# Performance work log

Hardware: AMD Instinct MI355X
Metric: run time of the kernel (lower is better)

## Reference

```python
import jax, jax.numpy as jnp
import numpy as np

B, S, D, H, MLP_D = 2, 2048, 512, 8, 128
DH = D // H  # 64
EPS = 1e-5


def setup_inputs() -> dict:
    key = jax.random.key(0)
    ks = jax.random.split(key, 8)
    return {
        "z": jax.random.normal(ks[0], (B, S, D), dtype=jnp.float32),
        "head_w": jax.random.normal(ks[1], (H, D, 3 * DH), dtype=jnp.float32),
        "w_o": jax.random.normal(ks[2], (H * DH, D), dtype=jnp.float32),
        "ln_w": jnp.ones((D,), dtype=jnp.float32),
        "ln_b": jnp.zeros((D,), dtype=jnp.float32),
        "w1": jax.random.normal(ks[3], (D, MLP_D), dtype=jnp.float32) * (1.0 / np.sqrt(D)),
        "b1": jnp.zeros((MLP_D,), dtype=jnp.float32),
        "w2": jax.random.normal(ks[4], (MLP_D, D), dtype=jnp.float32) * (1.0 / np.sqrt(MLP_D)),
        "b2": jnp.zeros((D,), dtype=jnp.float32),
    }


def _layernorm(x, w, b):
    mu = jnp.mean(x, axis=-1, keepdims=True)
    var = jnp.var(x, axis=-1, keepdims=True)
    return (x - mu) * jax.lax.rsqrt(var + EPS) * w + b


def reference(z, head_w, w_o, ln_w, ln_b, w1, b1, w2, b2):
    # --- MSA block: z = MSA(LN(z)) + z ---
    x = _layernorm(z, ln_w, ln_b)                       # [B,S,D]
    qkv = jnp.einsum("bsd,hde->bhse", x, head_w)        # [B,H,S,3*DH]
    q, k, v = qkv[..., :DH], qkv[..., DH:2 * DH], qkv[..., 2 * DH:]
    scores = jnp.einsum("bhsd,bhtd->bhst", q, k) / jnp.sqrt(jnp.float32(DH))
    p = jax.nn.softmax(scores, axis=-1)                 # [B,H,S,S]
    o = jnp.einsum("bhst,bhtd->bhsd", p, v)             # [B,H,S,DH]
    # concat heads along last dim (head order matches torch.cat), then project
    o = jnp.transpose(o, (0, 2, 1, 3)).reshape(B, S, H * DH)
    z = o @ w_o + z
    # --- MLP block: z = GELU(Linear2(Linear1(LN(z)))) + z (GELU last, per Sequential) ---
    y = _layernorm(z, ln_w, ln_b)
    y = (y @ w1 + b1) @ w2 + b2
    z = jax.nn.gelu(y, approximate=False) + z
    return z
```

## Files before the change

kernel.cpp:

```cpp
#include <hip/hip_runtime.h>
#include <hip/hip_bf16.h>

typedef unsigned short u16;
typedef __attribute__((ext_vector_type(8))) short short8;
typedef __attribute__((ext_vector_type(8))) __bf16 bf16x8;
typedef __attribute__((ext_vector_type(4))) float f32x4;

#define DEV static __device__ __forceinline__

DEV float bf2f(u16 u) { unsigned v = ((unsigned)u) << 16; float f; __builtin_memcpy(&f, &v, 4); return f; }
DEV u16 f2bf(float f) {
  unsigned u; __builtin_memcpy(&u, &f, 4);
  unsigned lsb = (u >> 16) & 1;
  u += 0x7fffu + lsb;
  return (u16)(u >> 16);
}
DEV u16 tbf(float f) {
  unsigned u; __builtin_memcpy(&u, &f, 4);
  return (u16)(u >> 16);
}
DEV float exp2fast(float x) { return __builtin_amdgcn_exp2f(x); }
DEV f32x4 mfma16(short8 a, short8 b, f32x4 c) {
  return __builtin_amdgcn_mfma_f32_16x16x32_bf16(
      __builtin_bit_cast(bf16x8, a), __builtin_bit_cast(bf16x8, b), c, 0, 0, 0);
}
DEV short8 ld8(const u16* p) { return *(const short8*)p; }

__global__ void prep_all(const float* __restrict__ hw, const float* __restrict__ wo,
                         const float* __restrict__ w1, const float* __restrict__ w2,
                         u16* __restrict__ wqh, u16* __restrict__ wql,
                         u16* __restrict__ woT, u16* __restrict__ w1T, u16* __restrict__ w2T) {
  int idx = blockIdx.x * 256 + threadIdx.x;
  if (idx < 786432) {
    int e = idx % 192;
    int d = (idx / 192) % 512;
    int h = idx / (192 * 512);
    float v = hw[idx];
    int n = (e < 64) ? (h * 64 + e) : (e < 128) ? (512 + h * 64 + e - 64) : (1024 + h * 64 + e - 128);
    size_t oi = (size_t)n * 512 + d;
    u16 hh = f2bf(v);
    wqh[oi] = hh;
    if (e < 128) wql[oi] = f2bf(v - bf2f(hh));
  } else if (idx < 786432 + 262144) {
    int i = idx - 786432;
    int n = i % 512, k = i / 512;
    woT[(size_t)n * 512 + k] = f2bf(wo[i]);
  } else if (idx < 786432 + 262144 + 65536) {
    int i = idx - (786432 + 262144);
    int n = i % 128, k = i / 128;
    w1T[(size_t)n * 512 + k] = f2bf(w1[i]);
  } else if (idx < 786432 + 262144 + 131072) {
    int i = idx - (786432 + 262144 + 65536);
    int n = i % 512, k = i / 512;
    w2T[(size_t)n * 128 + k] = f2bf(w2[i]);
  }
}

__global__ __launch_bounds__(256) void ln_kernel(const float* __restrict__ in,
                                                 const float* __restrict__ w,
                                                 const float* __restrict__ bb,
                                                 u16* __restrict__ hi, u16* __restrict__ lo) {
  const int wv = threadIdx.x >> 6, lane = threadIdx.x & 63;
  const int row = blockIdx.x * 4 + wv;
  const float4* r = (const float4*)(in + (size_t)row * 512);
  float4 a0 = r[lane * 2], a1 = r[lane * 2 + 1];
  float s = a0.x + a0.y + a0.z + a0.w + a1.x + a1.y + a1.z + a1.w;
  float ss = a0.x * a0.x + a0.y * a0.y + a0.z * a0.z + a0.w * a0.w +
             a1.x * a1.x + a1.y * a1.y + a1.z * a1.z + a1.w * a1.w;
#pragma unroll
  for (int m = 1; m < 64; m <<= 1) { s += __shfl_xor(s, m); ss += __shfl_xor(ss, m); }
  float mu = s * (1.f / 512.f);
  float var = ss * (1.f / 512.f) - mu * mu;
  float rstd = rsqrtf(var + 1e-5f);
  const float4* wp = (const float4*)w + lane * 2;
  const float4* bp = (const float4*)bb + lane * 2;
  float4 w0 = wp[0], w1v = wp[1], b0 = bp[0], b1v = bp[1];
  float xv[8] = {a0.x, a0.y, a0.z, a0.w, a1.x, a1.y, a1.z, a1.w};
  float wv8[8] = {w0.x, w0.y, w0.z, w0.w, w1v.x, w1v.y, w1v.z, w1v.w};
  float bv8[8] = {b0.x, b0.y, b0.z, b0.w, b1v.x, b1v.y, b1v.z, b1v.w};
  short8 oh, ol;
#pragma unroll
  for (int i = 0; i < 8; i++) {
    float v = (xv[i] - mu) * rstd * wv8[i] + bv8[i];
    u16 hh = f2bf(v);
    oh[i] = (short)hh;
    ol[i] = (short)f2bf(v - bf2f(hh));
  }
  *(short8*)(hi + (size_t)row * 512 + lane * 8) = oh;
  *(short8*)(lo + (size_t)row * 512 + lane * 8) = ol;
}

__global__ __launch_bounds__(256) void gemm_qkv(const u16* __restrict__ Ah, const u16* __restrict__ Alo,
                                                const u16* __restrict__ Bh, const u16* __restrict__ Blo,
                                                u16* __restrict__ outh, u16* __restrict__ outl) {
  __shared__ __align__(16) u16 As[128][40], Asl[128][40], Bs[64][40], Bsl[64][40];
  const int tid = threadIdx.x, lane = tid & 63, wv = tid >> 6;
  const int wm = wv >> 1, wn = wv & 1, g = lane >> 4, r16 = lane & 15;
  const int bm = blockIdx.x * 128, bn = blockIdx.y * 64;
  const bool split = blockIdx.y < 16;
  short8 sA[2], sAl[2], sB, sBl;
  auto ldtile = [&](int kt) {
#pragma unroll
    for (int c = 0; c < 2; c++) {
      int ch = c * 256 + tid;
      sA[c] = ld8(Ah + (size_t)(bm + (ch >> 2)) * 512 + kt + (ch & 3) * 8);
      if (split) sAl[c] = ld8(Alo + (size_t)(bm + (ch >> 2)) * 512 + kt + (ch & 3) * 8);
    }
    sB = ld8(Bh + (size_t)(bn + (tid >> 2)) * 512 + kt + (tid & 3) * 8);
    if (split) sBl = ld8(Blo + (size_t)(bn + (tid >> 2)) * 512 + kt + (tid & 3) * 8);
  };
  f32x4 acc[4][2] = {};
  ldtile(0);
  for (int kt = 0; kt < 512; kt += 32) {
    __syncthreads();
#pragma unroll
    for (int c = 0; c < 2; c++) {
      int ch = c * 256 + tid;
      *(short8*)&As[ch >> 2][(ch & 3) * 8] = sA[c];
      if (split) *(short8*)&Asl[ch >> 2][(ch & 3) * 8] = sAl[c];
    }
    *(short8*)&Bs[tid >> 2][(tid & 3) * 8] = sB;
    if (split) *(short8*)&Bsl[tid >> 2][(tid & 3) * 8] = sBl;
    __syncthreads();
    if (kt + 32 < 512) ldtile(kt + 32);
    short8 af[4], bf_[2], afl[4], bfl[2];
#pragma unroll
    for (int mi = 0; mi < 4; mi++) af[mi] = *(const short8*)&As[wm * 64 + mi * 16 + r16][g * 8];
#pragma unroll
    for (int ni = 0; ni < 2; ni++) bf_[ni] = *(const short8*)&Bs[wn * 32 + ni * 16 + r16][g * 8];
    if (split) {
#pragma unroll
      for (int mi = 0; mi < 4; mi++) afl[mi] = *(const short8*)&Asl[wm * 64 + mi * 16 + r16][g * 8];
#pragma unroll
      for (int ni = 0; ni < 2; ni++) bfl[ni] = *(const short8*)&Bsl[wn * 32 + ni * 16 + r16][g * 8];
    }
#pragma unroll
    for (int mi = 0; mi < 4; mi++)
#pragma unroll
      for (int ni = 0; ni < 2; ni++) {
        acc[mi][ni] = mfma16(af[mi], bf_[ni], acc[mi][ni]);
        if (split) {
          acc[mi][ni] = mfma16(af[mi], bfl[ni], acc[mi][ni]);
          acc[mi][ni] = mfma16(afl[mi], bf_[ni], acc[mi][ni]);
        }
      }
  }
#pragma unroll
  for (int mi = 0; mi < 4; mi++)
#pragma unroll
    for (int ni = 0; ni < 2; ni++) {
      int col = bn + wn * 32 + ni * 16 + r16;
      int row0 = bm + wm * 64 + mi * 16 + g * 4;
#pragma unroll
      for (int j = 0; j < 4; j++) {
        size_t oi = (size_t)(row0 + j) * 1536 + col;
        float v = acc[mi][ni][j];
        u16 hh = f2bf(v);
        outh[oi] = hh;
        if (split) outl[oi] = f2bf(v - bf2f(hh));
      }
    }
}

template <int MF, int NF, int EPI>
__global__ __launch_bounds__(256) void gemm_g(const u16* __restrict__ A, const u16* __restrict__ BT,
                                              const float* __restrict__ res, const float* __restrict__ bias,
                                              u16* __restrict__ outb, float* __restrict__ outf,
                                              int N, int K) {
  constexpr int BM = 32 * MF, BN = 32 * NF;
  constexpr int CA = (BM * 4 + 255) / 256, CB = (BN * 4 + 255) / 256;
  __shared__ __align__(16) u16 As[BM][40], Bs[BN][40];
  const int tid = threadIdx.x, lane = tid & 63, wv = tid >> 6;
  const int wm = wv >> 1, wn = wv & 1, g = lane >> 4, r16 = lane & 15;
  const int bm = blockIdx.x * BM, bn = blockIdx.y * BN;
  short8 sA[CA], sB[CB];
  auto ldtile = [&](int kt) {
#pragma unroll
    for (int c = 0; c < CA; c++) {
      int ch = c * 256 + tid;
      if (ch < BM * 4) sA[c] = ld8(A + (size_t)(bm + (ch >> 2)) * K + kt + (ch & 3) * 8);
    }
#pragma unroll
    for (int c = 0; c < CB; c++) {
      int ch = c * 256 + tid;
      if (ch < BN * 4) sB[c] = ld8(BT + (size_t)(bn + (ch >> 2)) * K + kt + (ch & 3) * 8);
    }
  };
  f32x4 acc[MF][NF] = {};
  ldtile(0);
  for (int kt = 0; kt < K; kt += 32) {
    __syncthreads();
#pragma unroll
    for (int c = 0; c < CA; c++) {
      int ch = c * 256 + tid;
      if (ch < BM * 4) *(short8*)&As[ch >> 2][(ch & 3) * 8] = sA[c];
    }
#pragma unroll
    for (int c = 0; c < CB; c++) {
      int ch = c * 256 + tid;
      if (ch < BN * 4) *(short8*)&Bs[ch >> 2][(ch & 3) * 8] = sB[c];
    }
    __syncthreads();
    if (kt + 32 < K) ldtile(kt + 32);
    short8 af[MF], bf_[NF];
#pragma unroll
    for (int mi = 0; mi < MF; mi++) af[mi] = *(const short8*)&As[wm * 16 * MF + mi * 16 + r16][g * 8];
#pragma unroll
    for (int ni = 0; ni < NF; ni++) bf_[ni] = *(const short8*)&Bs[wn * 16 * NF + ni * 16 + r16][g * 8];
#pragma unroll
    for (int mi = 0; mi < MF; mi++)
#pragma unroll
      for (int ni = 0; ni < NF; ni++) acc[mi][ni] = mfma16(af[mi], bf_[ni], acc[mi][ni]);
  }
#pragma unroll
  for (int mi = 0; mi < MF; mi++)
#pragma unroll
    for (int ni = 0; ni < NF; ni++) {
      int col = bn + wn * 16 * NF + ni * 16 + r16;
      int row0 = bm + wm * 16 * MF + mi * 16 + g * 4;
#pragma unroll
      for (int j = 0; j < 4; j++) {
        size_t oi = (size_t)(row0 + j) * N + col;
        float v = acc[mi][ni][j];
        if (EPI == 1) {
          outf[oi] = v + res[oi];
        } else if (EPI == 2) {
          outb[oi] = f2bf(v + bias[col]);
        } else {
          float u = v + bias[col];
          float gl = 0.5f * u * (1.0f + erff(u * 0.70710678118f));
          outf[oi] = gl + res[oi];
        }
      }
    }
}

__global__ __launch_bounds__(256) void attn_kernel(const u16* __restrict__ qkv_hi,
                                                   const u16* __restrict__ qkv_lo,
                                                   u16* __restrict__ o) {
  constexpr int SK = 72, SV = 136, SP = 136;
  __shared__ __align__(16) u16 Kh[128 * SK], Kl[128 * SK], Vt[64 * SV];
  __shared__ __align__(16) u16 Pl[4][16 * SP];
  const int tid = threadIdx.x, lane = tid & 63, w = tid >> 6;
  const int g = lane >> 4, r16 = lane & 15;
  const int qb = blockIdx.x * 64;
  const int b = blockIdx.y >> 3, h = blockIdx.y & 7;
  const size_t bbase = (size_t)b * 2048 * 1536;
  const u16* Qh = qkv_hi + bbase + h * 64;
  const u16* Ql = qkv_lo + bbase + h * 64;
  const u16* KgH = qkv_hi + bbase + 512 + h * 64;
  const u16* KgL = qkv_lo + bbase + 512 + h * 64;
  const u16* Vg = qkv_hi + bbase + 1024 + h * 64;

  const int qrow = qb + w * 16 + r16;
  short8 qh[2], qlo[2];
#pragma unroll
  for (int ks = 0; ks < 2; ks++) {
    qh[ks] = ld8(Qh + (size_t)qrow * 1536 + ks * 32 + g * 8);
    qlo[ks] = ld8(Ql + (size_t)qrow * 1536 + ks * 32 + g * 8);
  }

  f32x4 oacc[4] = {};
  float m_r[4], l_r[4];
#pragma unroll
  for (int j = 0; j < 4; j++) { m_r[j] = -3e38f; l_r[j] = 0.f; }

  short8 kA[4], kB[4], vS[4];
  auto ldkv = [&](int kt) {
#pragma unroll
    for (int c = 0; c < 4; c++) {
      int ch = c * 256 + tid;
      int kr = ch >> 3, kc = (ch & 7) * 8;
      kA[c] = ld8(KgH + (size_t)(kt + kr) * 1536 + kc);
      kB[c] = ld8(KgL + (size_t)(kt + kr) * 1536 + kc);
    }
#pragma unroll
    for (int c = 0; c < 2; c++)
#pragma unroll
      for (int c2 = 0; c2 < 2; c2++)
        vS[c * 2 + c2] = ld8(Vg + (size_t)(kt + c * 64 + lane) * 1536 + w * 16 + c2 * 8);
  };
  ldkv(0);

  for (int kt = 0; kt < 2048; kt += 128) {
    __syncthreads();
#pragma unroll
    for (int c = 0; c < 4; c++) {
      int ch = c * 256 + tid;
      int kr = ch >> 3, kc = (ch & 7) * 8;
      *(short8*)&Kh[kr * SK + kc] = kA[c];
      *(short8*)&Kl[kr * SK + kc] = kB[c];
    }
#pragma unroll
    for (int c = 0; c < 2; c++)
#pragma unroll
      for (int c2 = 0; c2 < 2; c2++)
#pragma unroll
        for (int i = 0; i < 8; i++)
          Vt[(w * 16 + c2 * 8 + i) * SV + c * 64 + lane] = (u16)vS[c * 2 + c2][i];
    __syncthreads();
    if (kt + 128 < 2048) ldkv(kt + 128);
    f32x4 s[8];
#pragma unroll
    for (int f = 0; f < 8; f++) {
      s[f] = f32x4{0.f, 0.f, 0.f, 0.f};
#pragma unroll
      for (int ks = 0; ks < 2; ks++) {
        short8 bh = *(const short8*)&Kh[(f * 16 + r16) * SK + ks * 32 + g * 8];
        short8 bl = *(const short8*)&Kl[(f * 16 + r16) * SK + ks * 32 + g * 8];
        s[f] = mfma16(qh[ks], bh, s[f]);
        s[f] = mfma16(qh[ks], bl, s[f]);
        s[f] = mfma16(qlo[ks], bh, s[f]);
      }
    }
    constexpr float SCL2 = 0.125f * 1.44269504f;
    float scl[4];
#pragma unroll
    for (int j = 0; j < 4; j++) {
      float a[8];
#pragma unroll
      for (int f = 0; f < 8; f++) a[f] = s[f][j] * SCL2;
      float vm = fmaxf(fmaxf(fmaxf(a[0], a[1]), fmaxf(a[2], a[3])),
                       fmaxf(fmaxf(a[4], a[5]), fmaxf(a[6], a[7])));
      vm = fmaxf(vm, __shfl_xor(vm, 1));
      vm = fmaxf(vm, __shfl_xor(vm, 2));
      vm = fmaxf(vm, __shfl_xor(vm, 4));
      vm = fmaxf(vm, __shfl_xor(vm, 8));
      float mn = fmaxf(m_r[j], vm);
      float rs = 0.f;
      int pr = (g * 4 + j) * SP + r16;
#pragma unroll
      for (int f = 0; f < 8; f++) {
        float e = exp2fast(a[f] - mn);
        rs += e;
        Pl[w][pr + f * 16] = tbf(e);
      }
      rs += __shfl_xor(rs, 1);
      rs += __shfl_xor(rs, 2);
      rs += __shfl_xor(rs, 4);
      rs += __shfl_xor(rs, 8);
      scl[j] = exp2fast(m_r[j] - mn);
      m_r[j] = mn;
      l_r[j] = l_r[j] * scl[j] + rs;
    }
#pragma unroll
    for (int dt = 0; dt < 4; dt++)
#pragma unroll
      for (int j = 0; j < 4; j++) oacc[dt][j] *= scl[j];
#pragma unroll
    for (int ks = 0; ks < 4; ks++) {
      short8 pa = *(const short8*)&Pl[w][r16 * SP + ks * 32 + g * 8];
#pragma unroll
      for (int dt = 0; dt < 4; dt++) {
        short8 vb = *(const short8*)&Vt[(dt * 16 + r16) * SV + ks * 32 + g * 8];
        oacc[dt] = mfma16(pa, vb, oacc[dt]);
      }
    }
  }
  float il[4];
#pragma unroll
  for (int j = 0; j < 4; j++) il[j] = 1.f / l_r[j];
#pragma unroll
  for (int dt = 0; dt < 4; dt++)
#pragma unroll
    for (int j = 0; j < 4; j++) {
      int row = b * 2048 + qb + w * 16 + g * 4 + j;
      int col = h * 64 + dt * 16 + r16;
      o[(size_t)row * 512 + col] = f2bf(oacc[dt][j] * il[j]);
    }
}

extern "C" void kernel_launch(void* const* d_in, const int* in_sizes, int n_in,
                              void* d_out, int out_size, void* d_ws, size_t ws_size,
                              hipStream_t stream) {
  const float* z = (const float*)d_in[0];
  const float* head_w = (const float*)d_in[1];
  const float* w_o = (const float*)d_in[2];
  const float* ln_w = (const float*)d_in[3];
  const float* ln_b = (const float*)d_in[4];
  const float* w1 = (const float*)d_in[5];
  const float* b1 = (const float*)d_in[6];
  const float* w2 = (const float*)d_in[7];
  const float* b2 = (const float*)d_in[8];
  float* out = (float*)d_out;

  size_t off = 0;
  auto alc = [&](size_t n) {
    void* p = (char*)d_ws + off;
    off += (n + 255) & ~(size_t)255;
    return p;
  };
  u16* x_hi = (u16*)alc((size_t)4096 * 512 * 2);
  u16* x_lo = (u16*)alc((size_t)4096 * 512 * 2);
  u16* wqh = (u16*)alc((size_t)1536 * 512 * 2);
  u16* wql = (u16*)alc((size_t)1536 * 512 * 2);
  u16* woT = (u16*)alc((size_t)512 * 512 * 2);
  u16* w1T = (u16*)alc((size_t)128 * 512 * 2);
  u16* w2T = (u16*)alc((size_t)512 * 128 * 2);
  u16* qkvh = (u16*)alc((size_t)4096 * 1536 * 2);
  u16* qkvl = (u16*)alc((size_t)4096 * 1536 * 2);
  u16* ob = (u16*)alc((size_t)4096 * 512 * 2);
  float* z2 = (float*)alc((size_t)4096 * 512 * 4);
  u16* tb = (u16*)alc((size_t)4096 * 128 * 2);

  prep_all<<<4608, 256, 0, stream>>>(head_w, w_o, w1, w2, wqh, wql, woT, w1T, w2T);

  ln_kernel<<<1024, 256, 0, stream>>>(z, ln_w, ln_b, x_hi, x_lo);

  gemm_qkv<<<dim3(32, 24), 256, 0, stream>>>(x_hi, x_lo, wqh, wql, qkvh, qkvl);

  attn_kernel<<<dim3(32, 16), 256, 0, stream>>>(qkvh, qkvl, ob);

  gemm_g<2, 2, 1><<<dim3(64, 8), 256, 0, stream>>>(ob, woT, z, nullptr, nullptr, z2, 512, 512);

  ln_kernel<<<1024, 256, 0, stream>>>(z2, ln_w, ln_b, x_hi, x_lo);

  gemm_g<1, 2, 2><<<dim3(128, 2), 256, 0, stream>>>(x_hi, w1T, nullptr, b1, tb, nullptr, 128, 512);

  gemm_g<2, 2, 3><<<dim3(64, 8), 256, 0, stream>>>(tb, w2T, z2, b2, nullptr, out, 512, 128);
}
```

Before: 144.5 us.

## Split attention KV range across two wave groups per block and merge results

The attention kernel now launches 512 threads per block, and each half of the waves processes half of the key/value sequence with 64-row tiles. At the end, the two partial softmax states are merged through shared memory. This doubles the waves working on each query tile, so more latency can be hidden on a grid of only 512 blocks. The cost is an extra merge step and shared-memory exchange, plus higher register pressure under launch bounds of 512 threads and 4 blocks.

```diff
diff --git a/kernel.cpp b/kernel.cpp
--- a/kernel.cpp
+++ b/kernel.cpp
@@ -235,13 +235,12 @@
     }
 }
 
-__global__ __launch_bounds__(256) void attn_kernel(const u16* __restrict__ qkv_hi,
-                                                   const u16* __restrict__ qkv_lo,
-                                                   u16* __restrict__ o) {
-  constexpr int SK = 72, SV = 136, SP = 136;
-  __shared__ __align__(16) u16 Kh[128 * SK], Kl[128 * SK], Vt[64 * SV];
-  __shared__ __align__(16) u16 Pl[4][16 * SP];
+__global__ __launch_bounds__(512, 4) void attn_kernel(const u16* __restrict__ qkv_hi,
+                                                      const u16* __restrict__ qkv_lo,
+                                                      u16* __restrict__ ob) {
+  __shared__ __align__(16) u16 smem[36864];
   const int tid = threadIdx.x, lane = tid & 63, w = tid >> 6;
+  const int half = w >> 2, wq = w & 3;
   const int g = lane >> 4, r16 = lane & 15;
   const int qb = blockIdx.x * 64;
   const int b = blockIdx.y >> 3, h = blockIdx.y & 7;
@@ -251,8 +250,12 @@
   const u16* KgH = qkv_hi + bbase + 512 + h * 64;
   const u16* KgL = qkv_lo + bbase + 512 + h * 64;
   const u16* Vg = qkv_hi + bbase + 1024 + h * 64;
-
-  const int qrow = qb + w * 16 + r16;
+  u16* Kh = smem + half * 4608;
+  u16* Kl = smem + 9216 + half * 4608;
+  u16* Vt = smem + 18432 + half * 4608;
+  u16* Pw = smem + 27648 + w * 1152;
+
+  const int qrow = qb + wq * 16 + r16;
   short8 qh[2], qlo[2];
 #pragma unroll
   for (int ks = 0; ks < 2; ks++) {
@@ -265,49 +268,44 @@
 #pragma unroll
   for (int j = 0; j < 4; j++) { m_r[j] = -3e38f; l_r[j] = 0.f; }
 
-  short8 kA[4], kB[4], vS[4];
+  const int th = tid & 255;
+  const int sr = th >> 2, sc16 = (th & 3) * 16;
+  const int kv0 = half * 1024;
+  short8 kA[2], kB[2], vS[2];
   auto ldkv = [&](int kt) {
-#pragma unroll
-    for (int c = 0; c < 4; c++) {
-      int ch = c * 256 + tid;
-      int kr = ch >> 3, kc = (ch & 7) * 8;
-      kA[c] = ld8(KgH + (size_t)(kt + kr) * 1536 + kc);
-      kB[c] = ld8(KgL + (size_t)(kt + kr) * 1536 + kc);
-    }
+    const u16* kp = KgH + (size_t)(kt + sr) * 1536 + sc16;
+    const u16* lp = KgL + (size_t)(kt + sr) * 1536 + sc16;
+    kA[0] = ld8(kp);
+    kA[1] = ld8(kp + 8);
+    kB[0] = ld8(lp);
+    kB[1] = ld8(lp + 8);
+    vS[0] = ld8(Vg + (size_t)(kt + lane) * 1536 + wq * 16);
+    vS[1] = ld8(Vg + (size_t)(kt + lane) * 1536 + wq * 16 + 8);
+  };
+  ldkv(kv0);
+
+  for (int kt = kv0; kt < kv0 + 1024; kt += 64) {
+    __syncthreads();
+    *(short8*)&Kh[sr * 72 + sc16] = kA[0];
+    *(short8*)&Kh[sr * 72 + sc16 + 8] = kA[1];
+    *(short8*)&Kl[sr * 72 + sc16] = kB[0];
+    *(short8*)&Kl[sr * 72 + sc16 + 8] = kB[1];
 #pragma unroll
     for (int c = 0; c < 2; c++)
 #pragma unroll
-      for (int c2 = 0; c2 < 2; c2++)
-        vS[c * 2 + c2] = ld8(Vg + (size_t)(kt + c * 64 + lane) * 1536 + w * 16 + c2 * 8);
-  };
-  ldkv(0);
-
-  for (int kt = 0; kt < 2048; kt += 128) {
-    __syncthreads();
-#pragma unroll
-    for (int c = 0; c < 4; c++) {
-      int ch = c * 256 + tid;
-      int kr = ch >> 3, kc = (ch & 7) * 8;
-      *(short8*)&Kh[kr * SK + kc] = kA[c];
-      *(short8*)&Kl[kr * SK + kc] = kB[c];
-    }
-#pragma unroll
-    for (int c = 0; c < 2; c++)
-#pragma unroll
-      for (int c2 = 0; c2 < 2; c2++)
-#pragma unroll
-        for (int i = 0; i < 8; i++)
-          Vt[(w * 16 + c2 * 8 + i) * SV + c * 64 + lane] = (u16)vS[c * 2 + c2][i];
-    __syncthreads();
-    if (kt + 128 < 2048) ldkv(kt + 128);
-    f32x4 s[8];
-#pragma unroll
-    for (int f = 0; f < 8; f++) {
+      for (int i = 0; i < 8; i++)
+        Vt[(wq * 16 + c * 8 + i) * 72 + lane] = (u16)vS[c][i];
+    __syncthreads();
+    if (kt + 64 < kv0 + 1024) ldkv(kt + 64);
+    f32x4 s[4];
+#pragma unroll
+    for (int f = 0; f < 4; f++) {
       s[f] = f32x4{0.f, 0.f, 0.f, 0.f};
+      int krow = f * 16 + r16;
 #pragma unroll
       for (int ks = 0; ks < 2; ks++) {
-        short8 bh = *(const short8*)&Kh[(f * 16 + r16) * SK + ks * 32 + g * 8];
-        short8 bl = *(const short8*)&Kl[(f * 16 + r16) * SK + ks * 32 + g * 8];
+        short8 bh = *(const short8*)&Kh[krow * 72 + ks * 32 + g * 8];
+        short8 bl = *(const short8*)&Kl[krow * 72 + ks * 32 + g * 8];
         s[f] = mfma16(qh[ks], bh, s[f]);
         s[f] = mfma16(qh[ks], bl, s[f]);
         s[f] = mfma16(qlo[ks], bh, s[f]);
@@ -317,24 +315,17 @@
     float scl[4];
 #pragma unroll
     for (int j = 0; j < 4; j++) {
-      float a[8];
-#pragma unroll
-      for (int f = 0; f < 8; f++) a[f] = s[f][j] * SCL2;
-      float vm = fmaxf(fmaxf(fmaxf(a[0], a[1]), fmaxf(a[2], a[3])),
-                       fmaxf(fmaxf(a[4], a[5]), fmaxf(a[6], a[7])));
+      float a0 = s[0][j] * SCL2, a1 = s[1][j] * SCL2;
+      float a2 = s[2][j] * SCL2, a3 = s[3][j] * SCL2;
+      float vm = fmaxf(fmaxf(a0, a1), fmaxf(a2, a3));
       vm = fmaxf(vm, __shfl_xor(vm, 1));
       vm = fmaxf(vm, __shfl_xor(vm, 2));
       vm = fmaxf(vm, __shfl_xor(vm, 4));
       vm = fmaxf(vm, __shfl_xor(vm, 8));
       float mn = fmaxf(m_r[j], vm);
-      float rs = 0.f;
-      int pr = (g * 4 + j) * SP + r16;
-#pragma unroll
-      for (int f = 0; f < 8; f++) {
-        float e = exp2fast(a[f] - mn);
-        rs += e;
-        Pl[w][pr + f * 16] = tbf(e);
-      }
+      float e0 = exp2fast(a0 - mn), e1 = exp2fast(a1 - mn);
+      float e2 = exp2fast(a2 - mn), e3 = exp2fast(a3 - mn);
+      float rs = (e0 + e1) + (e2 + e3);
       rs += __shfl_xor(rs, 1);
       rs += __shfl_xor(rs, 2);
       rs += __shfl_xor(rs, 4);
@@ -342,32 +333,63 @@
       scl[j] = exp2fast(m_r[j] - mn);
       m_r[j] = mn;
       l_r[j] = l_r[j] * scl[j] + rs;
+      int pr = (g * 4 + j) * 72 + r16;
+      Pw[pr] = tbf(e0);
+      Pw[pr + 16] = tbf(e1);
+      Pw[pr + 32] = tbf(e2);
+      Pw[pr + 48] = tbf(e3);
     }
 #pragma unroll
     for (int dt = 0; dt < 4; dt++)
 #pragma unroll
       for (int j = 0; j < 4; j++) oacc[dt][j] *= scl[j];
 #pragma unroll
-    for (int ks = 0; ks < 4; ks++) {
-      short8 pa = *(const short8*)&Pl[w][r16 * SP + ks * 32 + g * 8];
+    for (int ks = 0; ks < 2; ks++) {
+      short8 pa = *(const short8*)&Pw[r16 * 72 + ks * 32 + g * 8];
 #pragma unroll
       for (int dt = 0; dt < 4; dt++) {
-        short8 vb = *(const short8*)&Vt[(dt * 16 + r16) * SV + ks * 32 + g * 8];
+        short8 vb = *(const short8*)&Vt[(dt * 16 + r16) * 72 + ks * 32 + g * 8];
         oacc[dt] = mfma16(pa, vb, oacc[dt]);
       }
     }
   }
-  float il[4];
-#pragma unroll
-  for (int j = 0; j < 4; j++) il[j] = 1.f / l_r[j];
-#pragma unroll
-  for (int dt = 0; dt < 4; dt++)
+  __syncthreads();
+  float* oex = (float*)smem;
+  float* mlx = (float*)(smem + 9216);
+  if (half == 1) {
+#pragma unroll
+    for (int dt = 0; dt < 4; dt++)
+#pragma unroll
+      for (int j = 0; j < 4; j++)
+        oex[(wq * 16 + g * 4 + j) * 68 + dt * 16 + r16] = oacc[dt][j];
+    if (r16 == 0) {
+#pragma unroll
+      for (int j = 0; j < 4; j++) {
+        mlx[(wq * 16 + g * 4 + j) * 2] = m_r[j];
+        mlx[(wq * 16 + g * 4 + j) * 2 + 1] = l_r[j];
+      }
+    }
+  }
+  __syncthreads();
+  if (half == 0) {
 #pragma unroll
     for (int j = 0; j < 4; j++) {
-      int row = b * 2048 + qb + w * 16 + g * 4 + j;
-      int col = h * 64 + dt * 16 + r16;
-      o[(size_t)row * 512 + col] = f2bf(oacc[dt][j] * il[j]);
-    }
+      int rr = wq * 16 + g * 4 + j;
+      float m1 = mlx[rr * 2], l1 = mlx[rr * 2 + 1];
+      float mm = fmaxf(m_r[j], m1);
+      float c0 = exp2fast(m_r[j] - mm), c1 = exp2fast(m1 - mm);
+      float inv = 1.f / (c0 * l_r[j] + c1 * l1);
+      c0 *= inv;
+      c1 *= inv;
+      int row = b * 2048 + qb + rr;
+#pragma unroll
+      for (int dt = 0; dt < 4; dt++) {
+        float o1 = oex[rr * 68 + dt * 16 + r16];
+        int col = h * 64 + dt * 16 + r16;
+        ob[(size_t)row * 512 + col] = f2bf(oacc[dt][j] * c0 + o1 * c1);
+      }
+    }
+  }
 }
 
 extern "C" void kernel_launch(void* const* d_in, const int* in_sizes, int n_in,
@@ -409,7 +431,7 @@
 
   gemm_qkv<<<dim3(32, 24), 256, 0, stream>>>(x_hi, x_lo, wqh, wql, qkvh, qkvl);
 
-  attn_kernel<<<dim3(32, 16), 256, 0, stream>>>(qkvh, qkvl, ob);
+  attn_kernel<<<dim3(32, 16), 512, 0, stream>>>(qkvh, qkvl, ob);
 
   gemm_g<2, 2, 1><<<dim3(64, 8), 256, 0, stream>>>(ob, woT, z, nullptr, nullptr, z2, 512, 512);
 
```

Result: slower. 151.2 us (+4.6%).

## Emit V transposed from QKV GEMM so attention loads it with vector stores

Applied to the files above, without the earlier changes.

The QKV GEMM epilogue now writes Q/K hi/lo into a compact 1024-wide buffer and writes V transposed ([512 dims][4096 tokens]) as packed 4-element stores. The attention kernel then loads V rows contiguously along the key axis and stores them to LDS with 16-byte vector writes, replacing the per-element scatter transpose. This removes scalar LDS writes and strided global loads in the attention inner loop. In exchange, the GEMM writes V with a 4096-element stride between columns, which scatters its stores.

```diff
diff --git a/kernel.cpp b/kernel.cpp
--- a/kernel.cpp
+++ b/kernel.cpp
@@ -92,7 +92,8 @@
 
 __global__ __launch_bounds__(256) void gemm_qkv(const u16* __restrict__ Ah, const u16* __restrict__ Alo,
                                                 const u16* __restrict__ Bh, const u16* __restrict__ Blo,
-                                                u16* __restrict__ outh, u16* __restrict__ outl) {
+                                                u16* __restrict__ qkh, u16* __restrict__ qkl,
+                                                u16* __restrict__ vT) {
   __shared__ __align__(16) u16 As[128][40], Asl[128][40], Bs[64][40], Bsl[64][40];
   const int tid = threadIdx.x, lane = tid & 63, wv = tid >> 6;
   const int wm = wv >> 1, wn = wv & 1, g = lane >> 4, r16 = lane & 15;
@@ -151,13 +152,23 @@
     for (int ni = 0; ni < 2; ni++) {
       int col = bn + wn * 32 + ni * 16 + r16;
       int row0 = bm + wm * 64 + mi * 16 + g * 4;
-#pragma unroll
-      for (int j = 0; j < 4; j++) {
-        size_t oi = (size_t)(row0 + j) * 1536 + col;
-        float v = acc[mi][ni][j];
-        u16 hh = f2bf(v);
-        outh[oi] = hh;
-        if (split) outl[oi] = f2bf(v - bf2f(hh));
+      if (split) {
+#pragma unroll
+        for (int j = 0; j < 4; j++) {
+          size_t oi = (size_t)(row0 + j) * 1024 + col;
+          float v = acc[mi][ni][j];
+          u16 hh = f2bf(v);
+          qkh[oi] = hh;
+          qkl[oi] = f2bf(v - bf2f(hh));
+        }
+      } else {
+        int vcol = col - 1024;
+        ushort4 pk;
+        pk.x = f2bf(acc[mi][ni][0]);
+        pk.y = f2bf(acc[mi][ni][1]);
+        pk.z = f2bf(acc[mi][ni][2]);
+        pk.w = f2bf(acc[mi][ni][3]);
+        *(ushort4*)(vT + (size_t)vcol * 4096 + row0) = pk;
       }
     }
 }
@@ -235,8 +246,9 @@
     }
 }
 
-__global__ __launch_bounds__(256) void attn_kernel(const u16* __restrict__ qkv_hi,
-                                                   const u16* __restrict__ qkv_lo,
+__global__ __launch_bounds__(256) void attn_kernel(const u16* __restrict__ qkh,
+                                                   const u16* __restrict__ qkl,
+                                                   const u16* __restrict__ vT,
                                                    u16* __restrict__ o) {
   constexpr int SK = 72, SV = 136, SP = 136;
   __shared__ __align__(16) u16 Kh[128 * SK], Kl[128 * SK], Vt[64 * SV];
@@ -245,19 +257,19 @@
   const int g = lane >> 4, r16 = lane & 15;
   const int qb = blockIdx.x * 64;
   const int b = blockIdx.y >> 3, h = blockIdx.y & 7;
-  const size_t bbase = (size_t)b * 2048 * 1536;
-  const u16* Qh = qkv_hi + bbase + h * 64;
-  const u16* Ql = qkv_lo + bbase + h * 64;
-  const u16* KgH = qkv_hi + bbase + 512 + h * 64;
-  const u16* KgL = qkv_lo + bbase + 512 + h * 64;
-  const u16* Vg = qkv_hi + bbase + 1024 + h * 64;
+  const size_t bbase = (size_t)b * 2048 * 1024;
+  const u16* Qh = qkh + bbase + h * 64;
+  const u16* Ql = qkl + bbase + h * 64;
+  const u16* KgH = qkh + bbase + 512 + h * 64;
+  const u16* KgL = qkl + bbase + 512 + h * 64;
+  const u16* Vtg = vT + (size_t)h * 64 * 4096 + (size_t)b * 2048;
 
   const int qrow = qb + w * 16 + r16;
   short8 qh[2], qlo[2];
 #pragma unroll
   for (int ks = 0; ks < 2; ks++) {
-    qh[ks] = ld8(Qh + (size_t)qrow * 1536 + ks * 32 + g * 8);
-    qlo[ks] = ld8(Ql + (size_t)qrow * 1536 + ks * 32 + g * 8);
+    qh[ks] = ld8(Qh + (size_t)qrow * 1024 + ks * 32 + g * 8);
+    qlo[ks] = ld8(Ql + (size_t)qrow * 1024 + ks * 32 + g * 8);
   }
 
   f32x4 oacc[4] = {};
@@ -265,20 +277,19 @@
 #pragma unroll
   for (int j = 0; j < 4; j++) { m_r[j] = -3e38f; l_r[j] = 0.f; }
 
+  const int vd0 = tid >> 4, vkv = (tid & 15) * 8;
   short8 kA[4], kB[4], vS[4];
   auto ldkv = [&](int kt) {
 #pragma unroll
     for (int c = 0; c < 4; c++) {
       int ch = c * 256 + tid;
       int kr = ch >> 3, kc = (ch & 7) * 8;
-      kA[c] = ld8(KgH + (size_t)(kt + kr) * 1536 + kc);
-      kB[c] = ld8(KgL + (size_t)(kt + kr) * 1536 + kc);
-    }
-#pragma unroll
-    for (int c = 0; c < 2; c++)
-#pragma unroll
-      for (int c2 = 0; c2 < 2; c2++)
-        vS[c * 2 + c2] = ld8(Vg + (size_t)(kt + c * 64 + lane) * 1536 + w * 16 + c2 * 8);
+      kA[c] = ld8(KgH + (size_t)(kt + kr) * 1024 + kc);
+      kB[c] = ld8(KgL + (size_t)(kt + kr) * 1024 + kc);
+    }
+#pragma unroll
+    for (int c = 0; c < 4; c++)
+      vS[c] = ld8(Vtg + (size_t)(vd0 + c * 16) * 4096 + kt + vkv);
   };
   ldkv(0);
 
@@ -292,12 +303,8 @@
       *(short8*)&Kl[kr * SK + kc] = kB[c];
     }
 #pragma unroll
-    for (int c = 0; c < 2; c++)
-#pragma unroll
-      for (int c2 = 0; c2 < 2; c2++)
-#pragma unroll
-        for (int i = 0; i < 8; i++)
-          Vt[(w * 16 + c2 * 8 + i) * SV + c * 64 + lane] = (u16)vS[c * 2 + c2][i];
+    for (int c = 0; c < 4; c++)
+      *(short8*)&Vt[(vd0 + c * 16) * SV + vkv] = vS[c];
     __syncthreads();
     if (kt + 128 < 2048) ldkv(kt + 128);
     f32x4 s[8];
@@ -397,8 +404,9 @@
   u16* woT = (u16*)alc((size_t)512 * 512 * 2);
   u16* w1T = (u16*)alc((size_t)128 * 512 * 2);
   u16* w2T = (u16*)alc((size_t)512 * 128 * 2);
-  u16* qkvh = (u16*)alc((size_t)4096 * 1536 * 2);
-  u16* qkvl = (u16*)alc((size_t)4096 * 1536 * 2);
+  u16* qkh = (u16*)alc((size_t)4096 * 1024 * 2);
+  u16* qkl = (u16*)alc((size_t)4096 * 1024 * 2);
+  u16* vT = (u16*)alc((size_t)512 * 4096 * 2);
   u16* ob = (u16*)alc((size_t)4096 * 512 * 2);
   float* z2 = (float*)alc((size_t)4096 * 512 * 4);
   u16* tb = (u16*)alc((size_t)4096 * 128 * 2);
@@ -407,9 +415,9 @@
 
   ln_kernel<<<1024, 256, 0, stream>>>(z, ln_w, ln_b, x_hi, x_lo);
 
-  gemm_qkv<<<dim3(32, 24), 256, 0, stream>>>(x_hi, x_lo, wqh, wql, qkvh, qkvl);
-
-  attn_kernel<<<dim3(32, 16), 256, 0, stream>>>(qkvh, qkvl, ob);
+  gemm_qkv<<<dim3(32, 24), 256, 0, stream>>>(x_hi, x_lo, wqh, wql, qkh, qkl, vT);
+
+  attn_kernel<<<dim3(32, 16), 256, 0, stream>>>(qkh, qkl, vT, ob);
 
   gemm_g<2, 2, 1><<<dim3(64, 8), 256, 0, stream>>>(ob, woT, z, nullptr, nullptr, z2, 512, 512);
 
```

New measurement: 137.6 us. -4.8%, faster.
